# Kernel optimization log

Measured on AMD Instinct MI355X. Metric: run time of the kernel, lower is better.

## Reference

```python
import jax, jax.numpy as jnp
import numpy as np

SEQ_LEN, BATCH, INPUT_SIZE, HIDDEN_SIZE = 2048, 64, 512, 512


def _xavier_uniform(key, shape, dtype=jnp.float32):
    fan_out, fan_in = shape
    limit = float(np.sqrt(6.0 / (fan_in + fan_out)))
    return jax.random.uniform(key, shape, dtype, -limit, limit)


def setup_inputs() -> dict:
    key = jax.random.key(0)
    kx, kh, kW, kU, kb1, kb2 = jax.random.split(key, 6)
    x = jax.random.normal(kx, (SEQ_LEN, BATCH, INPUT_SIZE), dtype=jnp.float32)
    prev_hidden = jax.random.normal(kh, (BATCH, HIDDEN_SIZE), dtype=jnp.float32)
    W = _xavier_uniform(kW, (HIDDEN_SIZE, INPUT_SIZE))
    U = _xavier_uniform(kU, (HIDDEN_SIZE, HIDDEN_SIZE))
    # torch nn.init.uniform_ default is U(0, 1)
    hidden_bias = jax.random.uniform(kb1, (HIDDEN_SIZE,), dtype=jnp.float32)
    input_bias = jax.random.uniform(kb2, (HIDDEN_SIZE,), dtype=jnp.float32)
    return {"x": x, "prev_hidden": prev_hidden, "W": W, "U": U,
            "hidden_bias": hidden_bias, "input_bias": input_bias}


def reference(x, prev_hidden, W, U, hidden_bias, input_bias):
    # Faithful to the source: the loop never updates `prev_hidden`, so the
    # recurrent term U @ h0 + b_h is CONSTANT across timesteps and each
    # output is out_t = tanh(W x_t + b_in + U h0 + b_h). This vectorizes
    # into one batched GEMM over all timesteps plus a broadcast add.
    # x: (T, B, I); W: (H, I); U: (H, H)
    wx = jnp.einsum('tbi,hi->tbh', x, W) + input_bias          # (T, B, H)
    uh = prev_hidden @ U.T + hidden_bias                        # (B, H)
    outputs = jnp.tanh(wx + uh[None, :, :])                     # (T, B, H)
    hidden = outputs[-1]                                        # (B, H)
    return outputs, hidden
```

## Files before the change

### kernel.cpp

```cpp
#include <hip/hip_runtime.h>
#include <hip/hip_bf16.h>
#include <cstdint>
#include <cstddef>


#define T_LEN 2048
#define BATCH 64
#define ISZ 512
#define HSZ 512
#define MTOT (T_LEN * BATCH)

#define BM 128
#define BN 128
#define BK 64
#define NMT (MTOT / BM)

typedef __attribute__((ext_vector_type(8))) __bf16 bf16x8;
typedef __attribute__((ext_vector_type(4))) __bf16 bf16x4;
typedef __attribute__((ext_vector_type(4))) float f32x4;

#define GLOBAL_AS __attribute__((address_space(1)))
#define LDS_AS __attribute__((address_space(3)))

__device__ __forceinline__ float fast_tanh(float v) {
    float e = __expf(2.0f * v);
    return 1.0f - 2.0f / (e + 1.0f);
}

__global__ __launch_bounds__(256) void convw_kernel(const float* __restrict__ W,
                                                    __bf16* __restrict__ Wbf) {
    int i = blockIdx.x * 256 + threadIdx.x;
    f32x4 f = ((const f32x4*)W)[i];
    bf16x4 v;
    v[0] = (__bf16)f[0]; v[1] = (__bf16)f[1];
    v[2] = (__bf16)f[2]; v[3] = (__bf16)f[3];
    ((bf16x4*)Wbf)[i] = v;
}

__global__ __launch_bounds__(512) void uh_kernel(const float* __restrict__ prev,
                                                 const float* __restrict__ U,
                                                 const float* __restrict__ hb,
                                                 const float* __restrict__ ib,
                                                 float* __restrict__ uh) {
    __shared__ float sp[HSZ];
    int b = blockIdx.x, h = threadIdx.x;
    sp[h] = prev[b * HSZ + h];
    __syncthreads();
    const float* urow = U + (size_t)h * HSZ;
    float acc = 0.f;
#pragma unroll 4
    for (int i = 0; i < HSZ; i += 4) {
        f32x4 u4 = *(const f32x4*)(urow + i);
        acc += u4[0] * sp[i] + u4[1] * sp[i + 1] + u4[2] * sp[i + 2] + u4[3] * sp[i + 3];
    }
    uh[b * HSZ + h] = acc + hb[h] + ib[h];
}

__global__ __launch_bounds__(256) void gemm_tanh_kernel(
        const float* __restrict__ x, const __bf16* __restrict__ Wbf,
        const float* __restrict__ uh, float* __restrict__ out,
        float* __restrict__ hid) {
    __shared__ __attribute__((aligned(16))) __bf16 sA[2][BM * BK];
    __shared__ __attribute__((aligned(16))) __bf16 sB[2][BN * BK];

    int orig = blockIdx.x;
    int wg = (orig & 7) * 512 + (orig >> 3);
    int mt = wg >> 2, nt = wg & 3;

    int tid = threadIdx.x;
    int lane = tid & 63, wid = tid >> 6;
    int wr = wid >> 1, wc = wid & 1;
    int l15 = lane & 15, l4 = lane >> 4;

    const size_t m0 = (size_t)mt * BM;
    const int n0 = nt * BN;

    f32x4 acc[4][4] = {};
    f32x4 aPre[8];

    auto stageB = [&](int buf, int ks) {
#pragma unroll
        for (int j = 0; j < 4; ++j) {
            int chunk = wid * 4 + j;
            int row = chunk * 8 + (lane >> 3);
            int cb = ((lane & 7) ^ (lane >> 3)) << 4;
            const __bf16* g = Wbf + (size_t)(n0 + row) * ISZ + ks + (cb >> 1);
            __builtin_amdgcn_global_load_lds((const GLOBAL_AS uint32_t*)g,
                (LDS_AS uint32_t*)((char*)sB[buf] + chunk * 1024), 16, 0, 0);
        }
    };
    auto loadA = [&](int ks) {
#pragma unroll
        for (int it = 0; it < 4; ++it) {
            int p = it * 256 + tid;
            int row = p >> 3, pc = p & 7;
            const float* src = x + (m0 + row) * ISZ + ks + pc * 8;
            aPre[2 * it]     = *(const f32x4*)src;
            aPre[2 * it + 1] = *(const f32x4*)(src + 4);
        }
    };
    auto writeA = [&](int buf) {
#pragma unroll
        for (int it = 0; it < 4; ++it) {
            int p = it * 256 + tid;
            int row = p >> 3, pc = p & 7;
            f32x4 f0 = aPre[2 * it], f1 = aPre[2 * it + 1];
            bf16x8 v;
            v[0] = (__bf16)f0[0]; v[1] = (__bf16)f0[1];
            v[2] = (__bf16)f0[2]; v[3] = (__bf16)f0[3];
            v[4] = (__bf16)f1[0]; v[5] = (__bf16)f1[1];
            v[6] = (__bf16)f1[2]; v[7] = (__bf16)f1[3];
            int cb = (pc * 16) ^ ((row & 7) << 4);
            *(bf16x8*)((char*)sA[buf] + row * 128 + cb) = v;
        }
    };
    auto compute = [&](int buf) {
#pragma unroll
        for (int kk = 0; kk < 2; ++kk) {
            bf16x8 af[4], bfr[4];
#pragma unroll
            for (int mi = 0; mi < 4; ++mi) {
                int row = wr * 64 + mi * 16 + l15;
                int cb = (kk * 64 + l4 * 16) ^ ((row & 7) << 4);
                af[mi] = *(const bf16x8*)((const char*)sA[buf] + row * 128 + cb);
            }
#pragma unroll
            for (int ni = 0; ni < 4; ++ni) {
                int row = wc * 64 + ni * 16 + l15;
                int cb = (kk * 64 + l4 * 16) ^ ((row & 7) << 4);
                bfr[ni] = *(const bf16x8*)((const char*)sB[buf] + row * 128 + cb);
            }
#pragma unroll
            for (int mi = 0; mi < 4; ++mi)
#pragma unroll
                for (int ni = 0; ni < 4; ++ni)
                    acc[mi][ni] = __builtin_amdgcn_mfma_f32_16x16x32_bf16(
                        bfr[ni], af[mi], acc[mi][ni], 0, 0, 0);
        }
    };

    stageB(0, 0);
    loadA(0);
    writeA(0);
    __syncthreads();

#pragma unroll 2
    for (int t = 0; t < 7; ++t) {
        int cur = t & 1, nxt = cur ^ 1;
        int ks = (t + 1) * BK;
        loadA(ks);
        stageB(nxt, ks);
        compute(cur);
        writeA(nxt);
        __syncthreads();
    }
    compute(1);

    bool lastTile = (mt == NMT - 1);
#pragma unroll
    for (int mi = 0; mi < 4; ++mi) {
        int ml = wr * 64 + mi * 16 + l15;
        size_t m = m0 + ml;
        int bb = ml & 63;
#pragma unroll
        for (int ni = 0; ni < 4; ++ni) {
            int nb = n0 + wc * 64 + ni * 16 + l4 * 4;
            f32x4 u4 = *(const f32x4*)&uh[bb * HSZ + nb];
            f32x4 v;
#pragma unroll
            for (int r = 0; r < 4; ++r) v[r] = fast_tanh(acc[mi][ni][r] + u4[r]);
            *(f32x4*)&out[m * HSZ + nb] = v;
            if (lastTile && ml >= BM - BATCH)
                *(f32x4*)&hid[(size_t)(ml - (BM - BATCH)) * HSZ + nb] = v;
        }
    }
}

extern "C" void kernel_launch(void* const* d_in, const int* in_sizes, int n_in,
                              void* d_out, int out_size, void* d_ws, size_t ws_size,
                              hipStream_t stream) {
    const float* x  = (const float*)d_in[0];
    const float* ph = (const float*)d_in[1];
    const float* W  = (const float*)d_in[2];
    const float* U  = (const float*)d_in[3];
    const float* hb = (const float*)d_in[4];
    const float* ib = (const float*)d_in[5];
    float* out = (float*)d_out;
    float* hid = out + (size_t)MTOT * HSZ;

    __bf16* Wbf = (__bf16*)d_ws;
    float* uh   = (float*)((char*)d_ws + 512 * 1024);

    hipLaunchKernelGGL(convw_kernel, dim3(256), dim3(256), 0, stream, W, Wbf);
    hipLaunchKernelGGL(uh_kernel, dim3(64), dim3(512), 0, stream, ph, U, hb, ib, uh);
    hipLaunchKernelGGL(gemm_tanh_kernel, dim3(4096), dim3(256), 0, stream,
                       x, Wbf, uh, out, hid);
}
```

Measured before the change: 266.1 us.

## Single-buffer GEMM LDS for higher occupancy and merge prep kernels

Shared-memory tiles in the GEMM drop from double to single buffering, halving LDS use per block so more workgroups can be resident per CU. The main loop now prefetches A into registers, computes, then syncs twice around the LDS refill, and is no longer unrolled. The W bf16 conversion and U·h kernels are merged into one launch to remove a kernel launch. The cost is an extra barrier per k-step and less overlap of the B global-to-LDS load with compute within a block.

```diff
diff --git a/kernel.cpp b/kernel.cpp
--- a/kernel.cpp
+++ b/kernel.cpp
@@ -27,41 +27,42 @@
     return 1.0f - 2.0f / (e + 1.0f);
 }
 
-__global__ __launch_bounds__(256) void convw_kernel(const float* __restrict__ W,
-                                                    __bf16* __restrict__ Wbf) {
-    int i = blockIdx.x * 256 + threadIdx.x;
-    f32x4 f = ((const f32x4*)W)[i];
-    bf16x4 v;
-    v[0] = (__bf16)f[0]; v[1] = (__bf16)f[1];
-    v[2] = (__bf16)f[2]; v[3] = (__bf16)f[3];
-    ((bf16x4*)Wbf)[i] = v;
-}
-
-__global__ __launch_bounds__(512) void uh_kernel(const float* __restrict__ prev,
-                                                 const float* __restrict__ U,
-                                                 const float* __restrict__ hb,
-                                                 const float* __restrict__ ib,
-                                                 float* __restrict__ uh) {
-    __shared__ float sp[HSZ];
-    int b = blockIdx.x, h = threadIdx.x;
-    sp[h] = prev[b * HSZ + h];
-    __syncthreads();
-    const float* urow = U + (size_t)h * HSZ;
-    float acc = 0.f;
+__global__ __launch_bounds__(512) void prep_kernel(const float* __restrict__ W,
+                                                   __bf16* __restrict__ Wbf,
+                                                   const float* __restrict__ prev,
+                                                   const float* __restrict__ U,
+                                                   const float* __restrict__ hb,
+                                                   const float* __restrict__ ib,
+                                                   float* __restrict__ uh) {
+    if (blockIdx.x < 128) {
+        int i = blockIdx.x * 512 + threadIdx.x;
+        f32x4 f = ((const f32x4*)W)[i];
+        bf16x4 v;
+        v[0] = (__bf16)f[0]; v[1] = (__bf16)f[1];
+        v[2] = (__bf16)f[2]; v[3] = (__bf16)f[3];
+        ((bf16x4*)Wbf)[i] = v;
+    } else {
+        __shared__ float sp[HSZ];
+        int b = blockIdx.x - 128, h = threadIdx.x;
+        sp[h] = prev[b * HSZ + h];
+        __syncthreads();
+        const float* urow = U + (size_t)h * HSZ;
+        float acc = 0.f;
 #pragma unroll 4
-    for (int i = 0; i < HSZ; i += 4) {
-        f32x4 u4 = *(const f32x4*)(urow + i);
-        acc += u4[0] * sp[i] + u4[1] * sp[i + 1] + u4[2] * sp[i + 2] + u4[3] * sp[i + 3];
+        for (int i = 0; i < HSZ; i += 4) {
+            f32x4 u4 = *(const f32x4*)(urow + i);
+            acc += u4[0] * sp[i] + u4[1] * sp[i + 1] + u4[2] * sp[i + 2] + u4[3] * sp[i + 3];
+        }
+        uh[b * HSZ + h] = acc + hb[h] + ib[h];
     }
-    uh[b * HSZ + h] = acc + hb[h] + ib[h];
 }
 
 __global__ __launch_bounds__(256) void gemm_tanh_kernel(
         const float* __restrict__ x, const __bf16* __restrict__ Wbf,
         const float* __restrict__ uh, float* __restrict__ out,
         float* __restrict__ hid) {
-    __shared__ __attribute__((aligned(16))) __bf16 sA[2][BM * BK];
-    __shared__ __attribute__((aligned(16))) __bf16 sB[2][BN * BK];
+    __shared__ __attribute__((aligned(16))) __bf16 sA[BM * BK];
+    __shared__ __attribute__((aligned(16))) __bf16 sB[BN * BK];
 
     int orig = blockIdx.x;
     int wg = (orig & 7) * 512 + (orig >> 3);
@@ -78,7 +79,7 @@
     f32x4 acc[4][4] = {};
     f32x4 aPre[8];
 
-    auto stageB = [&](int buf, int ks) {
+    auto stageB = [&](int ks) {
 #pragma unroll
         for (int j = 0; j < 4; ++j) {
             int chunk = wid * 4 + j;
@@ -86,7 +87,7 @@
             int cb = ((lane & 7) ^ (lane >> 3)) << 4;
             const __bf16* g = Wbf + (size_t)(n0 + row) * ISZ + ks + (cb >> 1);
             __builtin_amdgcn_global_load_lds((const GLOBAL_AS uint32_t*)g,
-                (LDS_AS uint32_t*)((char*)sB[buf] + chunk * 1024), 16, 0, 0);
+                (LDS_AS uint32_t*)((char*)sB + chunk * 1024), 16, 0, 0);
         }
     };
     auto loadA = [&](int ks) {
@@ -99,7 +100,7 @@
             aPre[2 * it + 1] = *(const f32x4*)(src + 4);
         }
     };
-    auto writeA = [&](int buf) {
+    auto writeA = [&]() {
 #pragma unroll
         for (int it = 0; it < 4; ++it) {
             int p = it * 256 + tid;
@@ -111,10 +112,10 @@
             v[4] = (__bf16)f1[0]; v[5] = (__bf16)f1[1];
             v[6] = (__bf16)f1[2]; v[7] = (__bf16)f1[3];
             int cb = (pc * 16) ^ ((row & 7) << 4);
-            *(bf16x8*)((char*)sA[buf] + row * 128 + cb) = v;
+            *(bf16x8*)((char*)sA + row * 128 + cb) = v;
         }
     };
-    auto compute = [&](int buf) {
+    auto compute = [&]() {
 #pragma unroll
         for (int kk = 0; kk < 2; ++kk) {
             bf16x8 af[4], bfr[4];
@@ -122,13 +123,13 @@
             for (int mi = 0; mi < 4; ++mi) {
                 int row = wr * 64 + mi * 16 + l15;
                 int cb = (kk * 64 + l4 * 16) ^ ((row & 7) << 4);
-                af[mi] = *(const bf16x8*)((const char*)sA[buf] + row * 128 + cb);
+                af[mi] = *(const bf16x8*)((const char*)sA + row * 128 + cb);
             }
 #pragma unroll
             for (int ni = 0; ni < 4; ++ni) {
                 int row = wc * 64 + ni * 16 + l15;
                 int cb = (kk * 64 + l4 * 16) ^ ((row & 7) << 4);
-                bfr[ni] = *(const bf16x8*)((const char*)sB[buf] + row * 128 + cb);
+                bfr[ni] = *(const bf16x8*)((const char*)sB + row * 128 + cb);
             }
 #pragma unroll
             for (int mi = 0; mi < 4; ++mi)
@@ -139,22 +140,22 @@
         }
     };
 
-    stageB(0, 0);
     loadA(0);
-    writeA(0);
+    stageB(0);
+    writeA();
     __syncthreads();
 
-#pragma unroll 2
-    for (int t = 0; t < 7; ++t) {
-        int cur = t & 1, nxt = cur ^ 1;
-        int ks = (t + 1) * BK;
-        loadA(ks);
-        stageB(nxt, ks);
-        compute(cur);
-        writeA(nxt);
-        __syncthreads();
+#pragma unroll 1
+    for (int t = 0; t < 8; ++t) {
+        if (t < 7) loadA((t + 1) * BK);
+        compute();
+        if (t < 7) {
+            __syncthreads();
+            stageB((t + 1) * BK);
+            writeA();
+            __syncthreads();
+        }
     }
-    compute(1);
 
     bool lastTile = (mt == NMT - 1);
 #pragma unroll
@@ -191,8 +192,8 @@
     __bf16* Wbf = (__bf16*)d_ws;
     float* uh   = (float*)((char*)d_ws + 512 * 1024);
 
-    hipLaunchKernelGGL(convw_kernel, dim3(256), dim3(256), 0, stream, W, Wbf);
-    hipLaunchKernelGGL(uh_kernel, dim3(64), dim3(512), 0, stream, ph, U, hb, ib, uh);
+    hipLaunchKernelGGL(prep_kernel, dim3(192), dim3(512), 0, stream,
+                       W, Wbf, ph, U, hb, ib, uh);
     hipLaunchKernelGGL(gemm_tanh_kernel, dim3(4096), dim3(256), 0, stream,
                        x, Wbf, uh, out, hid);
 }
```

New measurement: 240.5 us. 1.11x faster.
